# Kernel optimization log

Hardware: AMD Instinct MI355X
Metric: run time of the kernel (lower is better)

Reference implementation:

```python
import jax, jax.numpy as jnp
import numpy as np

B, D = 256, 8                 # trees, tree depth (leaves at level D)
V, E, H = 32000, 128, 128     # vocab, embedding_dim, hidden_dim
N = 2 ** (D + 1) - 1          # 511 heap-indexed nodes per tree


def setup_inputs() -> dict:
    key = jax.random.key(0)
    ks = jax.random.split(key, 9)
    s = 0.05  # keep gate pre-activations in a sane range
    return {
        "tokens": jax.random.randint(ks[0], (B, N), 0, V),
        "arity": jax.random.randint(ks[1], (B, 2 ** D - 1), 0, 2).astype(jnp.int32),
        "emb": jax.random.normal(ks[2], (V, E), dtype=jnp.float32) * s,
        "W": jax.random.normal(ks[3], (4, E, H), dtype=jnp.float32) * s,      # i,f,o,u
        "bW": jax.random.normal(ks[4], (4, H), dtype=jnp.float32) * s,
        "Ubin": jax.random.normal(ks[5], (5, 2 * H, H), dtype=jnp.float32) * s,  # i,f_l,f_r,o,u
        "bUbin": jax.random.normal(ks[6], (5, H), dtype=jnp.float32) * s,
        "Uun": jax.random.normal(ks[7], (4, H, H), dtype=jnp.float32) * s,    # i,f,o,u
        "bUun": jax.random.normal(ks[8], (4, H), dtype=jnp.float32) * s,
    }


def reference(tokens, arity, emb, W, bW, Ubin, bUbin, Uun, bUun):
    # Level-synchronous bottom-up Tree-LSTM over heap-indexed perfect trees.
    x = emb[tokens]  # [B, N, E] embedding gather for every node
    depth = int(np.log2(tokens.shape[1] + 1)) - 1

    # Leaves (level `depth`): h = tanh(W_u x + b_u), c = 0
    off = 2 ** depth - 1
    lx = x[:, off:]  # [B, 2^D, E]
    h = jnp.tanh(jnp.einsum('bne,eh->bnh', lx, W[3]) + bW[3])
    c = jnp.zeros_like(h)

    for l in range(depth - 1, -1, -1):
        o2, cnt = 2 ** l - 1, 2 ** l
        nx = x[:, o2:o2 + cnt]            # [B, cnt, E] this level's tokens
        h_l, h_r = h[:, ::2], h[:, 1::2]   # children (heap order)
        c_l, c_r = c[:, ::2], c[:, 1::2]

        # Shared input projections for all 4 gates, fused into one GEMM
        Wx = jnp.einsum('bne,geh->gbnh', nx, W) + bW[:, None, None, :]
        hcat = jnp.concatenate([h_l, h_r], axis=-1)  # [B, cnt, 2H]
        Ub = jnp.einsum('bnk,gkh->gbnh', hcat, Ubin) + bUbin[:, None, None, :]
        Uu = jnp.einsum('bnh,gha->gbna', h_l, Uun) + bUun[:, None, None, :]

        # Binary branch: i, f_l, f_r (shared W_f), o, u
        i_b = jax.nn.sigmoid(Wx[0] + Ub[0])
        f_lg = jax.nn.sigmoid(Wx[1] + Ub[1])
        f_rg = jax.nn.sigmoid(Wx[1] + Ub[2])
        o_b = jax.nn.sigmoid(Wx[2] + Ub[3])
        u_b = jnp.tanh(Wx[3] + Ub[4])
        c_b = i_b * u_b + f_lg * c_l + f_rg * c_r
        h_b = o_b * jnp.tanh(c_b)

        # Unary branch (child = left child)
        i_u = jax.nn.sigmoid(Wx[0] + Uu[0])
        f_u = jax.nn.sigmoid(Wx[1] + Uu[1])
        o_u = jax.nn.sigmoid(Wx[2] + Uu[2])
        u_u = jnp.tanh(Wx[3] + Uu[3])
        c_u = i_u * u_u + f_u * c_l
        h_u = o_u * jnp.tanh(c_u)

        m = (arity[:, o2:o2 + cnt] == 1)[..., None]  # True -> binary node
        h = jnp.where(m, h_b, h_u)
        c = jnp.where(m, c_b, c_u)

    return h[:, 0], c[:, 0]  # root (h, c), each [B, H]
```

## Files before the change

kernel.cpp:

```cpp
#include <hip/hip_runtime.h>
#include <hip/hip_bf16.h>

#define NTOK 511
#define NINT 255

typedef unsigned short u16;
typedef __attribute__((ext_vector_type(8))) short bf16x8;
typedef __attribute__((ext_vector_type(4))) float f32x4;

constexpr int OFF_FLAG = 0;
constexpr int OFF_WB   = 4;
constexpr int W3B = 294912;
constexpr int WB_ELEMS = 311296;
constexpr int OFF_BIAS = OFF_WB + WB_ELEMS / 2;
constexpr int BW4 = 0, BUB4 = 512, BUB1 = 1024, BUU4 = 1152, B3 = 1664;
constexpr int BIAS_FLOATS = 1792;
constexpr int OFF_ROOT  = OFF_BIAS + BIAS_FLOATS;
constexpr int OFF_CHUNK = OFF_ROOT + 65536;
constexpr long PER_TREE = 49152;

__device__ __forceinline__ float bf2f(__hip_bfloat16 v) { return __bfloat162float(v); }
__device__ __forceinline__ short f2s(float f) {
    __hip_bfloat16 b = __float2bfloat16(f);
    return *reinterpret_cast<short*>(&b);
}
__device__ __forceinline__ float sigm(float x) { return 1.0f / (1.0f + __expf(-x)); }
__device__ __forceinline__ float tanh_(float x) { return 1.0f - 2.0f / (__expf(2.0f * x) + 1.0f); }

__device__ __forceinline__ float ldf(const void* p, long idx, int isbf) {
    return isbf ? bf2f(((const __hip_bfloat16*)p)[idx]) : ((const float*)p)[idx];
}

__device__ __forceinline__ bf16x8 ldA(const void* p, long idx, int isbf) {
    if (isbf) return *(const bf16x8*)((const short*)p + idx);
    const float* f = (const float*)p + idx;
    float4 a = *(const float4*)f, b = *(const float4*)(f + 4);
    bf16x8 r;
    r[0] = f2s(a.x); r[1] = f2s(a.y); r[2] = f2s(a.z); r[3] = f2s(a.w);
    r[4] = f2s(b.x); r[5] = f2s(b.y); r[6] = f2s(b.z); r[7] = f2s(b.w);
    return r;
}

typedef const __attribute__((address_space(1))) unsigned int* gp1_t;
typedef __attribute__((address_space(3))) unsigned int* lp3_t;
__device__ __forceinline__ void stage16(const void* g, void* l) {
    __builtin_amdgcn_global_load_lds((gp1_t)g, (lp3_t)l, 16, 0, 0);
}

__global__ void detect_kernel(const void* W, float* ws) {
    if (threadIdx.x == 0 && blockIdx.x == 0) {
        const u16* u = (const u16*)W;
        int cnt = 0;
        for (int i = 0; i < 128; i += 2) {
            u16 x = u[i];
            int ex = (x >> 7) & 0xff;
            if (x == 0 || (ex >= 96 && ex <= 127)) cnt++;
        }
        ((int*)ws)[0] = (cnt >= 48) ? 1 : 0;
    }
}

__global__ __launch_bounds__(256) void repack_mfma(
    const void* W, const void* bW, const void* Ubin, const void* bUbin,
    const void* Uun, const void* bUun, float* ws)
{
    const int isbf = ((const int*)ws)[0];
    short* wb = (short*)(ws + OFF_WB);
    float* bias = ws + OFF_BIAS;
    int tid = blockIdx.x * blockDim.x + threadIdx.x;
    int nth = gridDim.x * blockDim.x;

    for (int idx = tid; idx < 294912; idx += nth) {
        int e = idx & 511, fjc = idx >> 9;
        int jc = fjc / 72, f = fjc - jc * 72;
        int lane = e >> 3, id8 = e & 7;
        int j = jc * 16 + (lane & 15);
        float v;
        if (f < 16) {
            int g = f >> 2, ks = f & 3;
            int k = ks * 32 + (lane >> 4) * 8 + id8;
            v = ldf(W, (long)g * 16384 + k * 128 + j, isbf);
        } else if (f < 32) {
            int fu = f - 16; int g = fu >> 2, ks = fu & 3;
            int k = ks * 32 + (lane >> 4) * 8 + id8;
            v = ldf(Uun, (long)g * 16384 + k * 128 + j, isbf);
        } else {
            int fb = f - 32; int g = fb >> 3, ks = fb & 7;
            int k = ks * 32 + (lane >> 4) * 8 + id8;
            v = ldf(Ubin, (long)g * 32768 + k * 128 + j, isbf);
        }
        wb[idx] = f2s(v);
    }
    for (int idx = tid; idx < 16384; idx += nth) {
        int e = idx & 511, frag = idx >> 9;
        int jc = frag >> 2, ks = frag & 3;
        int lane = e >> 3, id8 = e & 7;
        int k = ks * 32 + (lane >> 4) * 8 + id8;
        int j = jc * 16 + (lane & 15);
        wb[W3B + idx] = f2s(ldf(W, (long)3 * 16384 + k * 128 + j, isbf));
    }
    for (int j = tid; j < 128; j += nth) {
        float4 b;
        b.x = ldf(bW, 0 * 128 + j, isbf); b.y = ldf(bW, 1 * 128 + j, isbf);
        b.z = ldf(bW, 2 * 128 + j, isbf); b.w = ldf(bW, 3 * 128 + j, isbf);
        ((float4*)(bias + BW4))[j] = b;
        float4 bb;
        bb.x = ldf(bUbin, 0 * 128 + j, isbf); bb.y = ldf(bUbin, 1 * 128 + j, isbf);
        bb.z = ldf(bUbin, 2 * 128 + j, isbf); bb.w = ldf(bUbin, 3 * 128 + j, isbf);
        ((float4*)(bias + BUB4))[j] = bb;
        (bias + BUB1)[j] = ldf(bUbin, 4 * 128 + j, isbf);
        float4 bu;
        bu.x = ldf(bUun, 0 * 128 + j, isbf); bu.y = ldf(bUun, 1 * 128 + j, isbf);
        bu.z = ldf(bUun, 2 * 128 + j, isbf); bu.w = ldf(bUun, 3 * 128 + j, isbf);
        ((float4*)(bias + BUU4))[j] = bu;
        (bias + B3)[j] = ldf(bW, 3 * 128 + j, isbf);
    }
}

#define MFMA(A, B, C) __builtin_amdgcn_mfma_f32_16x16x32_bf16(A, B, C, 0, 0, 0)

__global__ __launch_bounds__(256, 2) void leaf_mfma(
    const int* __restrict__ tokens, const void* emb, const float* __restrict__ ws,
    short* __restrict__ hOut, int treeOff, int Mtot, int iters)
{
    __shared__ short hst[4][16][132];
    const int t = threadIdx.x;
    const int isbf = ((const int*)ws)[0];
    const int wv = t >> 6, lane = t & 63, quad = lane >> 4, l16 = lane & 15;
    const short* wb = (const short*)(ws + OFF_WB);
    const float* bias = ws + OFF_BIAS;

    bf16x8 bf[32];
#pragma unroll
    for (int f = 0; f < 32; ++f)
        bf[f] = *(const bf16x8*)(wb + W3B + f * 512 + lane * 8);
    float b3v[8];
#pragma unroll
    for (int jc = 0; jc < 8; ++jc) b3v[jc] = (bias + B3)[jc * 16 + l16];

    for (int it = 0; it < iters; ++it) {
        int rb = (blockIdx.x * iters + it) * 64 + wv * 16;
        if (rb >= Mtot) break;
        int p = rb + l16; if (p >= Mtot) p = Mtot - 1;
        int bl = p >> 8, i = p & 255;
        int tk = tokens[(long)(treeOff + bl) * NTOK + 255 + i];
        bf16x8 ax[4];
#pragma unroll
        for (int ks = 0; ks < 4; ++ks)
            ax[ks] = ldA(emb, (long)tk * 128 + ks * 32 + quad * 8, isbf);
        f32x4 acc[8];
#pragma unroll
        for (int jc = 0; jc < 8; ++jc) acc[jc] = {0.f, 0.f, 0.f, 0.f};
#pragma unroll
        for (int jc = 0; jc < 8; ++jc)
#pragma unroll
            for (int ks = 0; ks < 4; ++ks)
                acc[jc] = MFMA(ax[ks], bf[jc * 4 + ks], acc[jc]);
#pragma unroll
        for (int jc = 0; jc < 8; ++jc)
#pragma unroll
            for (int r = 0; r < 4; ++r)
                hst[wv][quad * 4 + r][jc * 16 + l16] = f2s(tanh_(acc[jc][r] + b3v[jc]));
        int nloc = lane >> 2, c0 = (lane & 3) * 4;
        int prow = rb + nloc;
        if (prow < Mtot) {
#pragma unroll
            for (int jcb = 0; jcb < 8; ++jcb) {
                uint2 v = *(const uint2*)&hst[wv][nloc][jcb * 16 + c0];
                *(uint2*)&hOut[((long)jcb * Mtot + prow) * 16 + c0] = v;
            }
        }
    }
}

__global__ __launch_bounds__(256, 2) void level2_mfma(
    const int* __restrict__ tokens, const int* __restrict__ arity, const void* emb,
    const float* __restrict__ ws, const short* __restrict__ hChild,
    const float* __restrict__ cChild, short* __restrict__ hOut, float* __restrict__ cOut,
    int lvl, int treeOff, int leafchild, int Mtot, int Mchild,
    int NBMB, int Q)
{
    __shared__ short Bs[72 * 512];
    __shared__ short hst[4][16][20];

    const int t = threadIdx.x;
    const int isbf = ((const int*)ws)[0];
    const int jc = blockIdx.x / NBMB;
    const int mb = blockIdx.x - jc * NBMB;
    const int wv = t >> 6, lane = t & 63, quad = lane >> 4, l16 = lane & 15;
    const int cnt = 1 << lvl, o2 = cnt - 1;
    const short* wb = (const short*)(ws + OFF_WB);
    const float* bias = ws + OFF_BIAS;
    const short* wj = wb + (long)jc * 36864;

#pragma unroll
    for (int s = 0; s < 18; ++s) {
        int off = (s * 256 + t) * 8;
        stage16(wj + off, Bs + off);
    }

    const int j = jc * 16 + l16;
    const float4 bw = ((const float4*)(bias + BW4))[j];
    const float4 bb = ((const float4*)(bias + BUB4))[j];
    const float  b1 = (bias + BUB1)[j];
    const float4 bu = ((const float4*)(bias + BUU4))[j];

    __syncthreads();

    for (int q = 0; q < Q; ++q) {
        const int p0 = (mb * Q + q) * 64;
        if (p0 >= Mtot) break;

        int row = wv * 16 + l16;
        int p = p0 + row; if (p >= Mtot) p = Mtot - 1;
        int bl = p >> lvl, i = p - (bl << lvl);
        long crow = (long)bl * (cnt << 1) + 2 * i;
        int tk = tokens[(long)(treeOff + bl) * NTOK + o2 + i];
        bf16x8 ax[4], ah[8];
#pragma unroll
        for (int ks = 0; ks < 4; ++ks)
            ax[ks] = ldA(emb, (long)tk * 128 + ks * 32 + quad * 8, isbf);
#pragma unroll
        for (int ks = 0; ks < 8; ++ks) {
            int k0 = ks * 32 + quad * 8;
            int side = k0 >> 7, kl = k0 & 127;
            ah[ks] = *(const bf16x8*)(hChild +
                ((long)(kl >> 4) * Mchild + crow + side) * 16 + (kl & 15));
        }

        f32x4 aW[4], aU[4], aB[5];
#pragma unroll
        for (int g = 0; g < 4; ++g) { aW[g] = {0,0,0,0}; aU[g] = {0,0,0,0}; }
#pragma unroll
        for (int g = 0; g < 5; ++g) aB[g] = {0,0,0,0};

#pragma unroll
        for (int f = 0; f < 16; ++f) {
            bf16x8 b = *(const bf16x8*)&Bs[f * 512 + lane * 8];
            aW[f >> 2] = MFMA(ax[f & 3], b, aW[f >> 2]);
        }
#pragma unroll
        for (int f = 16; f < 32; ++f) {
            bf16x8 b = *(const bf16x8*)&Bs[f * 512 + lane * 8];
            aU[(f - 16) >> 2] = MFMA(ah[(f - 16) & 3], b, aU[(f - 16) >> 2]);
        }
#pragma unroll
        for (int f = 32; f < 72; ++f) {
            bf16x8 b = *(const bf16x8*)&Bs[f * 512 + lane * 8];
            int fb = f - 32;
            aB[fb >> 3] = MFMA(ah[fb & 7], b, aB[fb >> 3]);
        }

        int arv[4]; float clv[4], crv[4];
#pragma unroll
        for (int r = 0; r < 4; ++r) {
            int pe = p0 + wv * 16 + quad * 4 + r;
            if (pe >= Mtot) pe = Mtot - 1;
            int ble = pe >> lvl, ie = pe - (ble << lvl);
            arv[r] = arity[(long)(treeOff + ble) * NINT + o2 + ie];
            if (!leafchild) {
                long crowe = (long)ble * (cnt << 1) + 2 * ie;
                clv[r] = cChild[((long)jc * Mchild + crowe) * 16 + l16];
                crv[r] = cChild[((long)jc * Mchild + crowe + 1) * 16 + l16];
            } else { clv[r] = 0.f; crv[r] = 0.f; }
        }

#pragma unroll
        for (int r = 0; r < 4; ++r) {
            int ml = wv * 16 + quad * 4 + r;
            int pr = p0 + ml;
            bool val = (pr < Mtot);
            int pc = val ? pr : Mtot - 1;
            bool bin = (arv[r] == 1);
            float w0 = aW[0][r] + bw.x;
            float w1 = aW[1][r] + bw.y;
            float w2 = aW[2][r] + bw.z;
            float w3 = aW[3][r] + bw.w;
            float pi, pf, po, pu;
            if (bin) { pi = w0 + aB[0][r] + bb.x; pf = w1 + aB[1][r] + bb.y;
                       po = w2 + aB[3][r] + bb.w; pu = w3 + aB[4][r] + b1; }
            else     { pi = w0 + aU[0][r] + bu.x; pf = w1 + aU[1][r] + bu.y;
                       po = w2 + aU[2][r] + bu.z; pu = w3 + aU[3][r] + bu.w; }
            float cl = clv[r];
            float cr = bin ? crv[r] : 0.f;
            float frv = bin ? sigm(w1 + aB[2][r] + bb.z) : 0.f;
            float ig = sigm(pi), fg = sigm(pf), og = sigm(po), ug = tanh_(pu);
            float c = ig * ug + fg * cl + frv * cr;
            float h = og * tanh_(c);
            if (val) cOut[((long)jc * Mtot + pc) * 16 + l16] = c;
            hst[wv][quad * 4 + r][l16] = f2s(h);
        }
        {
            int nloc = lane >> 2, c0 = (lane & 3) * 4;
            int prow = p0 + wv * 16 + nloc;
            if (prow < Mtot) {
                uint2 v = *(const uint2*)&hst[wv][nloc][c0];
                *(uint2*)&hOut[((long)jc * Mtot + prow) * 16 + c0] = v;
            }
        }
    }
}

__global__ __launch_bounds__(256, 2) void tail_mfma(
    const int* __restrict__ tokens, const int* __restrict__ arity, const void* emb,
    const float* __restrict__ ws, const short* __restrict__ hChild,
    const float* __restrict__ cChild, float* __restrict__ rootH, float* __restrict__ rootC,
    int treeOff, int Mchild4)
{
    __shared__ short hb[2][8 * 16 * 20];
    __shared__ float cb[2][8 * 16 * 20];

    const int t = threadIdx.x;
    const int isbf = ((const int*)ws)[0];
    const int bl = blockIdx.x;
    const int wv = t >> 6, lane = t & 63, quad = lane >> 4, l16 = lane & 15;
    const short* wb = (const short*)(ws + OFF_WB);
    const float* bias = ws + OFF_BIAS;
    const long tB = (long)(treeOff + bl) * NTOK;
    const long tA = (long)(treeOff + bl) * NINT;

    int cur = 0;
    for (int l = 4; l >= 0; --l) {
        const int cnt = 1 << l, o2 = cnt - 1;
        int i = (l16 < cnt) ? l16 : cnt - 1;
        int tk = tokens[tB + o2 + i];
        bf16x8 ax[4], ah[8];
#pragma unroll
        for (int ks = 0; ks < 4; ++ks)
            ax[ks] = ldA(emb, (long)tk * 128 + ks * 32 + quad * 8, isbf);
        if (l == 4) {
            long crow = (long)bl * 32 + 2 * i;
#pragma unroll
            for (int ks = 0; ks < 8; ++ks) {
                int k0 = ks * 32 + quad * 8, side = k0 >> 7, kl = k0 & 127;
                ah[ks] = *(const bf16x8*)(hChild +
                    ((long)(kl >> 4) * Mchild4 + crow + side) * 16 + (kl & 15));
            }
        } else {
            int crow = 2 * i;
#pragma unroll
            for (int ks = 0; ks < 8; ++ks) {
                int k0 = ks * 32 + quad * 8, side = k0 >> 7, kl = k0 & 127;
                ah[ks] = *(const bf16x8*)&hb[cur][(kl >> 4) * 320 + (crow + side) * 20 + (kl & 15)];
            }
        }
        for (int jx = 0; jx < 2; ++jx) {
            const int jc = wv * 2 + jx;
            const short* wj = wb + (long)jc * 36864;
            const int j = jc * 16 + l16;
            const float4 bw = ((const float4*)(bias + BW4))[j];
            const float4 bb = ((const float4*)(bias + BUB4))[j];
            const float  b1 = (bias + BUB1)[j];
            const float4 bu = ((const float4*)(bias + BUU4))[j];

            f32x4 aW[4], aU[4], aB[5];
#pragma unroll
            for (int g = 0; g < 4; ++g) { aW[g] = {0,0,0,0}; aU[g] = {0,0,0,0}; }
#pragma unroll
            for (int g = 0; g < 5; ++g) aB[g] = {0,0,0,0};

#pragma unroll
            for (int f = 0; f < 16; ++f) {
                bf16x8 b = *(const bf16x8*)(wj + f * 512 + lane * 8);
                aW[f >> 2] = MFMA(ax[f & 3], b, aW[f >> 2]);
            }
#pragma unroll
            for (int f = 16; f < 32; ++f) {
                bf16x8 b = *(const bf16x8*)(wj + f * 512 + lane * 8);
                aU[(f - 16) >> 2] = MFMA(ah[(f - 16) & 3], b, aU[(f - 16) >> 2]);
            }
#pragma unroll
            for (int f = 32; f < 72; ++f) {
                bf16x8 b = *(const bf16x8*)(wj + f * 512 + lane * 8);
                int fb = f - 32;
                aB[fb >> 3] = MFMA(ah[fb & 7], b, aB[fb >> 3]);
            }

#pragma unroll
            for (int r = 0; r < 4; ++r) {
                int node = quad * 4 + r;
                int ie = (node < cnt) ? node : cnt - 1;
                int arvv = arity[tA + o2 + ie];
                float cl, cr;
                if (l == 4) {
                    long crowe = (long)bl * 32 + 2 * ie;
                    cl = cChild[((long)jc * Mchild4 + crowe) * 16 + l16];
                    cr = cChild[((long)jc * Mchild4 + crowe + 1) * 16 + l16];
                } else {
                    int crowe = 2 * ie;
                    cl = cb[cur][jc * 320 + crowe * 20 + l16];
                    cr = cb[cur][jc * 320 + (crowe + 1) * 20 + l16];
                }
                bool bin = (arvv == 1);
                float w0 = aW[0][r] + bw.x;
                float w1 = aW[1][r] + bw.y;
                float w2 = aW[2][r] + bw.z;
                float w3 = aW[3][r] + bw.w;
                float pi, pf, po, pu;
                if (bin) { pi = w0 + aB[0][r] + bb.x; pf = w1 + aB[1][r] + bb.y;
                           po = w2 + aB[3][r] + bb.w; pu = w3 + aB[4][r] + b1; }
                else     { pi = w0 + aU[0][r] + bu.x; pf = w1 + aU[1][r] + bu.y;
                           po = w2 + aU[2][r] + bu.z; pu = w3 + aU[3][r] + bu.w; }
                if (!bin) cr = 0.f;
                float frv = bin ? sigm(w1 + aB[2][r] + bb.z) : 0.f;
                float ig = sigm(pi), fg = sigm(pf), og = sigm(po), ug = tanh_(pu);
                float c = ig * ug + fg * cl + frv * cr;
                float h = og * tanh_(c);
                if (l == 0) {
                    if (node == 0) {
                        rootH[(long)(treeOff + bl) * 128 + j] = h;
                        rootC[(long)(treeOff + bl) * 128 + j] = c;
                    }
                } else if (node < cnt) {
                    hb[cur ^ 1][jc * 320 + node * 20 + l16] = f2s(h);
                    cb[cur ^ 1][jc * 320 + node * 20 + l16] = c;
                }
            }
        }
        __syncthreads();
        cur ^= 1;
    }
}

__global__ __launch_bounds__(256) void out_kernel(const float* ws, void* out)
{
    const int isbf = ((const int*)ws)[0];
    const float* rootH = ws + OFF_ROOT;
    const float* rootC = rootH + 32768;
    int t = blockIdx.x * 256 + threadIdx.x;
    float h = rootH[t], c = rootC[t];
    if (isbf) {
        ((__hip_bfloat16*)out)[t]         = __float2bfloat16(h);
        ((__hip_bfloat16*)out)[32768 + t] = __float2bfloat16(c);
    } else {
        ((float*)out)[t]         = h;
        ((float*)out)[32768 + t] = c;
    }
}

extern "C" void kernel_launch(void* const* d_in, const int* in_sizes, int n_in,
                              void* d_out, int out_size, void* d_ws, size_t ws_size,
                              hipStream_t stream)
{
    const int* tokens = (const int*)d_in[0];
    const int* arity  = (const int*)d_in[1];
    const void* emb   = d_in[2];
    const void* W     = d_in[3];
    const void* bW    = d_in[4];
    const void* Ubin  = d_in[5];
    const void* bUbin = d_in[6];
    const void* Uun   = d_in[7];
    const void* bUun  = d_in[8];

    float* ws = (float*)d_ws;

    int Bc = 256;
    while (Bc > 1 && (size_t)(OFF_CHUNK + Bc * PER_TREE) * 4 > ws_size) Bc >>= 1;
    const int nCh = 256 / Bc;

    detect_kernel<<<1, 64, 0, stream>>>(W, ws);
    repack_mfma<<<128, 256, 0, stream>>>(W, bW, Ubin, bUbin, Uun, bUun, ws);

    short* Ha = (short*)(ws + OFF_CHUNK);
    short* Hb = Ha + (long)Bc * 32768;
    float* Ca = (float*)(Hb + (long)Bc * 16384);
    float* Cb = Ca + (long)Bc * 8192;
    float* rootH = ws + OFF_ROOT;
    float* rootC = rootH + 32768;

    for (int cidx = 0; cidx < nCh; ++cidx) {
        int toff = cidx * Bc;
        {
            int Mleaf = Bc * 256;
            int NBL = (Mleaf + 63) / 64; if (NBL > 512) NBL = 512;
            int itersL = (Mleaf + NBL * 64 - 1) / (NBL * 64);
            leaf_mfma<<<NBL, 256, 0, stream>>>(tokens, emb, ws, Ha, toff, Mleaf, itersL);
        }
        for (int l = 7; l >= 5; --l) {
            int M = Bc << l;
            int Mchild = Bc << (l + 1);
            const short* hC = (l & 1) ? Ha : Hb;
            const float* cC = (l & 1) ? Ca : Cb;
            short* hO = (l & 1) ? Hb : Ha;
            float* cO = (l & 1) ? Cb : Ca;
            int lc = (l == 7) ? 1 : 0;
            int NBM = (M + 63) / 64;
            int Q = (NBM + 127) / 128;
            int NBMB = (NBM + Q - 1) / Q;
            level2_mfma<<<dim3(NBMB * 8), 256, 0, stream>>>(
                tokens, arity, emb, ws, hC, cC, hO, cO,
                l, toff, lc, M, Mchild, NBMB, Q);
        }
        tail_mfma<<<dim3(Bc), 256, 0, stream>>>(
            tokens, arity, emb, ws, Hb, Cb, rootH, rootC, toff, Bc << 5);
    }
    out_kernel<<<128, 256, 0, stream>>>(ws, d_out);
}
```

Measured before the change: 183.5 us.

## Replace per-tree tail kernel with per-level launches spread across blocks

The single tail kernel, which ran levels 4..0 inside one block per tree and kept child state in shared memory, is replaced by one launch per level. Each launch spreads node rows and hidden chunks across many blocks, using the same global ping-pong buffers as the upper levels. This raises parallelism on the small top levels, where one block per tree left most of the device idle. In exchange it adds four more kernel launches and round trips through global memory between levels.

```diff
diff --git a/kernel.cpp b/kernel.cpp
--- a/kernel.cpp
+++ b/kernel.cpp
@@ -301,124 +301,125 @@
     }
 }
 
-__global__ __launch_bounds__(256, 2) void tail_mfma(
+__global__ __launch_bounds__(256, 2) void level_direct(
     const int* __restrict__ tokens, const int* __restrict__ arity, const void* emb,
     const float* __restrict__ ws, const short* __restrict__ hChild,
-    const float* __restrict__ cChild, float* __restrict__ rootH, float* __restrict__ rootC,
-    int treeOff, int Mchild4)
+    const float* __restrict__ cChild, short* __restrict__ hOut, float* __restrict__ cOut,
+    float* __restrict__ rootH, float* __restrict__ rootC,
+    int lvl, int treeOff, int isRoot, int Mtot, int Mchild, int NBM)
 {
-    __shared__ short hb[2][8 * 16 * 20];
-    __shared__ float cb[2][8 * 16 * 20];
+    __shared__ short hst[4][16][20];
 
     const int t = threadIdx.x;
     const int isbf = ((const int*)ws)[0];
-    const int bl = blockIdx.x;
+    const int jc = blockIdx.x / NBM;
+    const int mb = blockIdx.x - jc * NBM;
     const int wv = t >> 6, lane = t & 63, quad = lane >> 4, l16 = lane & 15;
+    const int cnt = 1 << lvl, o2 = cnt - 1;
     const short* wb = (const short*)(ws + OFF_WB);
     const float* bias = ws + OFF_BIAS;
-    const long tB = (long)(treeOff + bl) * NTOK;
-    const long tA = (long)(treeOff + bl) * NINT;
-
-    int cur = 0;
-    for (int l = 4; l >= 0; --l) {
-        const int cnt = 1 << l, o2 = cnt - 1;
-        int i = (l16 < cnt) ? l16 : cnt - 1;
-        int tk = tokens[tB + o2 + i];
-        bf16x8 ax[4], ah[8];
-#pragma unroll
-        for (int ks = 0; ks < 4; ++ks)
-            ax[ks] = ldA(emb, (long)tk * 128 + ks * 32 + quad * 8, isbf);
-        if (l == 4) {
-            long crow = (long)bl * 32 + 2 * i;
-#pragma unroll
-            for (int ks = 0; ks < 8; ++ks) {
-                int k0 = ks * 32 + quad * 8, side = k0 >> 7, kl = k0 & 127;
-                ah[ks] = *(const bf16x8*)(hChild +
-                    ((long)(kl >> 4) * Mchild4 + crow + side) * 16 + (kl & 15));
+    const short* wj = wb + (long)jc * 36864;
+
+    const int j = jc * 16 + l16;
+    const float4 bw = ((const float4*)(bias + BW4))[j];
+    const float4 bb = ((const float4*)(bias + BUB4))[j];
+    const float  b1 = (bias + BUB1)[j];
+    const float4 bu = ((const float4*)(bias + BUU4))[j];
+
+    const int p0 = mb * 64;
+
+    int row = wv * 16 + l16;
+    int p = p0 + row; if (p >= Mtot) p = Mtot - 1;
+    int bl = p >> lvl, i = p - (bl << lvl);
+    long crow = (long)bl * (cnt << 1) + 2 * i;
+    int tk = tokens[(long)(treeOff + bl) * NTOK + o2 + i];
+    bf16x8 ax[4], ah[8];
+#pragma unroll
+    for (int ks = 0; ks < 4; ++ks)
+        ax[ks] = ldA(emb, (long)tk * 128 + ks * 32 + quad * 8, isbf);
+#pragma unroll
+    for (int ks = 0; ks < 8; ++ks) {
+        int k0 = ks * 32 + quad * 8;
+        int side = k0 >> 7, kl = k0 & 127;
+        ah[ks] = *(const bf16x8*)(hChild +
+            ((long)(kl >> 4) * Mchild + crow + side) * 16 + (kl & 15));
+    }
+
+    f32x4 aW[4], aU[4], aB[5];
+#pragma unroll
+    for (int g = 0; g < 4; ++g) { aW[g] = {0,0,0,0}; aU[g] = {0,0,0,0}; }
+#pragma unroll
+    for (int g = 0; g < 5; ++g) aB[g] = {0,0,0,0};
+
+#pragma unroll
+    for (int f = 0; f < 16; ++f) {
+        bf16x8 b = *(const bf16x8*)(wj + f * 512 + lane * 8);
+        aW[f >> 2] = MFMA(ax[f & 3], b, aW[f >> 2]);
+    }
+#pragma unroll
+    for (int f = 16; f < 32; ++f) {
+        bf16x8 b = *(const bf16x8*)(wj + f * 512 + lane * 8);
+        aU[(f - 16) >> 2] = MFMA(ah[(f - 16) & 3], b, aU[(f - 16) >> 2]);
+    }
+#pragma unroll
+    for (int f = 32; f < 72; ++f) {
+        bf16x8 b = *(const bf16x8*)(wj + f * 512 + lane * 8);
+        int fb = f - 32;
+        aB[fb >> 3] = MFMA(ah[fb & 7], b, aB[fb >> 3]);
+    }
+
+    int arv[4]; float clv[4], crv[4];
+#pragma unroll
+    for (int r = 0; r < 4; ++r) {
+        int pe = p0 + wv * 16 + quad * 4 + r;
+        if (pe >= Mtot) pe = Mtot - 1;
+        int ble = pe >> lvl, ie = pe - (ble << lvl);
+        arv[r] = arity[(long)(treeOff + ble) * NINT + o2 + ie];
+        long crowe = (long)ble * (cnt << 1) + 2 * ie;
+        clv[r] = cChild[((long)jc * Mchild + crowe) * 16 + l16];
+        crv[r] = cChild[((long)jc * Mchild + crowe + 1) * 16 + l16];
+    }
+
+#pragma unroll
+    for (int r = 0; r < 4; ++r) {
+        int ml = wv * 16 + quad * 4 + r;
+        int pr = p0 + ml;
+        bool val = (pr < Mtot);
+        int pc = val ? pr : Mtot - 1;
+        int ble = pc >> lvl;
+        bool bin = (arv[r] == 1);
+        float w0 = aW[0][r] + bw.x;
+        float w1 = aW[1][r] + bw.y;
+        float w2 = aW[2][r] + bw.z;
+        float w3 = aW[3][r] + bw.w;
+        float pi, pf, po, pu;
+        if (bin) { pi = w0 + aB[0][r] + bb.x; pf = w1 + aB[1][r] + bb.y;
+                   po = w2 + aB[3][r] + bb.w; pu = w3 + aB[4][r] + b1; }
+        else     { pi = w0 + aU[0][r] + bu.x; pf = w1 + aU[1][r] + bu.y;
+                   po = w2 + aU[2][r] + bu.z; pu = w3 + aU[3][r] + bu.w; }
+        float cl = clv[r];
+        float cr = bin ? crv[r] : 0.f;
+        float frv = bin ? sigm(w1 + aB[2][r] + bb.z) : 0.f;
+        float ig = sigm(pi), fg = sigm(pf), og = sigm(po), ug = tanh_(pu);
+        float c = ig * ug + fg * cl + frv * cr;
+        float h = og * tanh_(c);
+        if (isRoot) {
+            if (val) {
+                rootH[(long)(treeOff + ble) * 128 + j] = h;
+                rootC[(long)(treeOff + ble) * 128 + j] = c;
             }
         } else {
-            int crow = 2 * i;
-#pragma unroll
-            for (int ks = 0; ks < 8; ++ks) {
-                int k0 = ks * 32 + quad * 8, side = k0 >> 7, kl = k0 & 127;
-                ah[ks] = *(const bf16x8*)&hb[cur][(kl >> 4) * 320 + (crow + side) * 20 + (kl & 15)];
-            }
-        }
-        for (int jx = 0; jx < 2; ++jx) {
-            const int jc = wv * 2 + jx;
-            const short* wj = wb + (long)jc * 36864;
-            const int j = jc * 16 + l16;
-            const float4 bw = ((const float4*)(bias + BW4))[j];
-            const float4 bb = ((const float4*)(bias + BUB4))[j];
-            const float  b1 = (bias + BUB1)[j];
-            const float4 bu = ((const float4*)(bias + BUU4))[j];
-
-            f32x4 aW[4], aU[4], aB[5];
-#pragma unroll
-            for (int g = 0; g < 4; ++g) { aW[g] = {0,0,0,0}; aU[g] = {0,0,0,0}; }
-#pragma unroll
-            for (int g = 0; g < 5; ++g) aB[g] = {0,0,0,0};
-
-#pragma unroll
-            for (int f = 0; f < 16; ++f) {
-                bf16x8 b = *(const bf16x8*)(wj + f * 512 + lane * 8);
-                aW[f >> 2] = MFMA(ax[f & 3], b, aW[f >> 2]);
-            }
-#pragma unroll
-            for (int f = 16; f < 32; ++f) {
-                bf16x8 b = *(const bf16x8*)(wj + f * 512 + lane * 8);
-                aU[(f - 16) >> 2] = MFMA(ah[(f - 16) & 3], b, aU[(f - 16) >> 2]);
-            }
-#pragma unroll
-            for (int f = 32; f < 72; ++f) {
-                bf16x8 b = *(const bf16x8*)(wj + f * 512 + lane * 8);
-                int fb = f - 32;
-                aB[fb >> 3] = MFMA(ah[fb & 7], b, aB[fb >> 3]);
-            }
-
-#pragma unroll
-            for (int r = 0; r < 4; ++r) {
-                int node = quad * 4 + r;
-                int ie = (node < cnt) ? node : cnt - 1;
-                int arvv = arity[tA + o2 + ie];
-                float cl, cr;
-                if (l == 4) {
-                    long crowe = (long)bl * 32 + 2 * ie;
-                    cl = cChild[((long)jc * Mchild4 + crowe) * 16 + l16];
-                    cr = cChild[((long)jc * Mchild4 + crowe + 1) * 16 + l16];
-                } else {
-                    int crowe = 2 * ie;
-                    cl = cb[cur][jc * 320 + crowe * 20 + l16];
-                    cr = cb[cur][jc * 320 + (crowe + 1) * 20 + l16];
-                }
-                bool bin = (arvv == 1);
-                float w0 = aW[0][r] + bw.x;
-                float w1 = aW[1][r] + bw.y;
-                float w2 = aW[2][r] + bw.z;
-                float w3 = aW[3][r] + bw.w;
-                float pi, pf, po, pu;
-                if (bin) { pi = w0 + aB[0][r] + bb.x; pf = w1 + aB[1][r] + bb.y;
-                           po = w2 + aB[3][r] + bb.w; pu = w3 + aB[4][r] + b1; }
-                else     { pi = w0 + aU[0][r] + bu.x; pf = w1 + aU[1][r] + bu.y;
-                           po = w2 + aU[2][r] + bu.z; pu = w3 + aU[3][r] + bu.w; }
-                if (!bin) cr = 0.f;
-                float frv = bin ? sigm(w1 + aB[2][r] + bb.z) : 0.f;
-                float ig = sigm(pi), fg = sigm(pf), og = sigm(po), ug = tanh_(pu);
-                float c = ig * ug + fg * cl + frv * cr;
-                float h = og * tanh_(c);
-                if (l == 0) {
-                    if (node == 0) {
-                        rootH[(long)(treeOff + bl) * 128 + j] = h;
-                        rootC[(long)(treeOff + bl) * 128 + j] = c;
-                    }
-                } else if (node < cnt) {
-                    hb[cur ^ 1][jc * 320 + node * 20 + l16] = f2s(h);
-                    cb[cur ^ 1][jc * 320 + node * 20 + l16] = c;
-                }
-            }
-        }
-        __syncthreads();
-        cur ^= 1;
+            if (val) cOut[((long)jc * Mtot + pc) * 16 + l16] = c;
+            hst[wv][quad * 4 + r][l16] = f2s(h);
+        }
+    }
+    if (!isRoot) {
+        int nloc = lane >> 2, c0 = (lane & 3) * 4;
+        int prow = p0 + wv * 16 + nloc;
+        if (prow < Mtot) {
+            uint2 v = *(const uint2*)&hst[wv][nloc][c0];
+            *(uint2*)&hOut[((long)jc * Mtot + prow) * 16 + c0] = v;
+        }
     }
 }
 
@@ -491,8 +492,19 @@
                 tokens, arity, emb, ws, hC, cC, hO, cO,
                 l, toff, lc, M, Mchild, NBMB, Q);
         }
-        tail_mfma<<<dim3(Bc), 256, 0, stream>>>(
-            tokens, arity, emb, ws, Hb, Cb, rootH, rootC, toff, Bc << 5);
+        for (int l = 4; l >= 0; --l) {
+            int M = Bc << l;
+            int Mchild = Bc << (l + 1);
+            const short* hC = (l & 1) ? Ha : Hb;
+            const float* cC = (l & 1) ? Ca : Cb;
+            short* hO = (l & 1) ? Hb : Ha;
+            float* cO = (l & 1) ? Cb : Ca;
+            int isRoot = (l == 0) ? 1 : 0;
+            int NBM = (M + 63) / 64;
+            level_direct<<<dim3(NBM * 8), 256, 0, stream>>>(
+                tokens, arity, emb, ws, hC, cC, hO, cO, rootH, rootC,
+                l, toff, isRoot, M, Mchild, NBM);
+        }
     }
     out_kernel<<<128, 256, 0, stream>>>(ws, d_out);
 }
```

After: 184.4 us. Within noise of the previous version (+0.5%).
